# Kernel tuning notes

Hardware: AMD Instinct MI355X
Metric: run time of the kernel (lower is better)

Reference implementation:

```python
import jax, jax.numpy as jnp
import numpy as np

NUM_ITERATIONS = 3
LAMBDA_WEIGHT = 0.6
EPS = 1e-8


def _squash(s):
    # s: [N, out_dim]; norm over feature dim (dim=1 in torch, keepdim)
    s_norm = jnp.linalg.norm(s, axis=1, keepdims=True)
    scale = s_norm / (1.0 + s_norm)
    return scale * s / (s_norm + EPS)


def setup_inputs() -> dict:
    key = jax.random.key(0)
    k_h, k_adj, k_w, k_a = jax.random.split(key, 4)
    N, in_dim, out_dim = 4096, 128, 128
    h = jax.random.normal(k_h, (N, in_dim), dtype=jnp.float32)
    adj = jax.random.uniform(k_adj, (N, N), dtype=jnp.float32)
    # xavier_uniform for W [in_dim, out_dim] and attn_a [2*out_dim, 1]
    lim_w = float(np.sqrt(6.0 / (in_dim + out_dim)))
    W = jax.random.uniform(k_w, (in_dim, out_dim), minval=-lim_w, maxval=lim_w, dtype=jnp.float32)
    lim_a = float(np.sqrt(6.0 / (2 * out_dim + 1)))
    attn_a = jax.random.uniform(k_a, (2 * out_dim, 1), minval=-lim_a, maxval=lim_a, dtype=jnp.float32)
    return {"h": h, "adj": adj, "W": W, "attn_a": attn_a}


def reference(h, adj, W, attn_a):
    # Symmetric degree normalization
    d = adj.sum(axis=1) + 1e-8
    d_inv_sqrt = 1.0 / jnp.sqrt(d)
    adj_norm = d_inv_sqrt[:, None] * adj * d_inv_sqrt[None, :]  # [N, N]

    u_hat = h @ W  # [N, out_dim]

    # GAT-style scores via additive decomposition (same math as cat+matmul,
    # avoids the O(N^2 * 2d) h_concat tensor):
    out_dim = W.shape[1]
    a_src = attn_a[:out_dim, 0]  # [in_dim] (in_dim == out_dim)
    a_dst = attn_a[out_dim:, 0]
    attn_scores = (h @ a_src)[:, None] + (h @ a_dst)[None, :]  # [N, N]
    attn_weights = jax.nn.leaky_relu(attn_scores, negative_slope=0.2)

    # Dynamic routing
    b = adj_norm
    c = None
    for it in range(NUM_ITERATIONS):
        c = jax.nn.softmax(b, axis=1)  # [N, N]
        s = c @ u_hat                  # [N, out_dim]
        v = _squash(s)
        if it < NUM_ITERATIONS - 1:
            b = b + v @ u_hat.T        # agreement [N, N]

    combined = LAMBDA_WEIGHT * c + (1.0 - LAMBDA_WEIGHT) * jax.nn.softmax(attn_weights, axis=1)
    s = combined @ u_hat
    return _squash(s)
```

## Files before the change

kernel.cpp:

```cpp
#include <hip/hip_runtime.h>
#include <hip/hip_bf16.h>
#include <math.h>

#define N 4096
#define D 128
#define EPSV 1e-8f
#define KS 8

typedef __attribute__((ext_vector_type(8))) short bf16x8;
typedef __attribute__((ext_vector_type(4))) float f32x4;

__device__ __forceinline__ float lrelu(float x){ return x > 0.f ? x : 0.2f*x; }

__device__ __forceinline__ ushort bf16_hi(float x){
  __hip_bfloat16 h = __float2bfloat16(x);
  return *reinterpret_cast<ushort*>(&h);
}
__device__ __forceinline__ float bf16_tof(ushort u){
  __hip_bfloat16 h = *reinterpret_cast<__hip_bfloat16*>(&u);
  return __bfloat162float(h);
}

__device__ __forceinline__ float wave_sum(float v){
  #pragma unroll
  for (int off = 32; off; off >>= 1) v += __shfl_down(v, off);
  return v;
}
__device__ __forceinline__ float wave_max(float v){
  #pragma unroll
  for (int off = 32; off; off >>= 1) v = fmaxf(v, __shfl_down(v, off));
  return v;
}
__device__ __forceinline__ float block_sum256(float v, float* red){
  v = wave_sum(v);
  if ((threadIdx.x & 63) == 0) red[threadIdx.x >> 6] = v;
  __syncthreads();
  float r = (red[0] + red[1]) + (red[2] + red[3]);
  __syncthreads();
  return r;
}
__device__ __forceinline__ float block_max256(float v, float* red){
  v = wave_max(v);
  if ((threadIdx.x & 63) == 0) red[threadIdx.x >> 6] = v;
  __syncthreads();
  float r = fmaxf(fmaxf(red[0], red[1]), fmaxf(red[2], red[3]));
  __syncthreads();
  return r;
}

__global__ void k_rowsum(const float* __restrict__ adj, float* __restrict__ dis){
  int i = blockIdx.x;
  const float4* row = reinterpret_cast<const float4*>(adj + (size_t)i * N);
  float s = 0.f;
  #pragma unroll
  for (int l = 0; l < 4; ++l){
    float4 v = row[threadIdx.x + l * 256];
    s += (v.x + v.y) + (v.z + v.w);
  }
  __shared__ float red[4];
  s = block_sum256(s, red);
  if (threadIdx.x == 0) dis[i] = 1.0f / sqrtf(s + EPSV);
}

__global__ void k_uhat2(const float* __restrict__ h, const float* __restrict__ W,
                        const float* __restrict__ aa,
                        ushort* __restrict__ u_hi, ushort* __restrict__ u_lo,
                        float* __restrict__ p, float* __restrict__ q){
  int i = blockIdx.x, t = threadIdx.x;
  __shared__ float hs[D];
  __shared__ float red[4];
  float hv = h[(size_t)i * D + t];
  hs[t] = hv;
  __syncthreads();
  float acc = 0.f;
  #pragma unroll 8
  for (int k = 0; k < D; ++k) acc = fmaf(hs[k], W[k * D + t], acc);
  ushort hh = bf16_hi(acc);
  u_hi[(size_t)i * D + t] = hh;
  u_lo[(size_t)i * D + t] = bf16_hi(acc - bf16_tof(hh));
  float pv = hv * aa[t];
  float qv = hv * aa[D + t];
  pv = wave_sum(pv); qv = wave_sum(qv);
  if ((t & 63) == 0){ red[t >> 6] = pv; red[2 + (t >> 6)] = qv; }
  __syncthreads();
  if (t == 0){ p[i] = red[0] + red[1]; q[i] = red[2] + red[3]; }
}

__global__ void k_transposeU(const ushort* __restrict__ u_hi, const ushort* __restrict__ u_lo,
                             ushort* __restrict__ uT_hi, ushort* __restrict__ uT_lo){
  __shared__ ushort T[64][136];
  const int tid = threadIdx.x;
  const int j0 = blockIdx.x * 64;
  for (int pass = 0; pass < 2; ++pass){
    const ushort* s = pass ? u_lo : u_hi;
    ushort* d = pass ? uT_lo : uT_hi;
    __syncthreads();
    #pragma unroll
    for (int l = 0; l < 4; ++l){
      int r = l * 16 + (tid >> 4);
      int c = (tid & 15) * 8;
      *reinterpret_cast<uint4*>(&T[r][c]) =
          *reinterpret_cast<const uint4*>(s + (size_t)(j0 + r) * D + c);
    }
    __syncthreads();
    const int dd = tid >> 1, half = tid & 1;
    ushort* drow = d + (size_t)dd * N + j0 + half * 32;
    #pragma unroll
    for (int m4 = 0; m4 < 8; ++m4){
      ushort4 w;
      w.x = T[half * 32 + m4 * 4 + 0][dd];
      w.y = T[half * 32 + m4 * 4 + 1][dd];
      w.z = T[half * 32 + m4 * 4 + 2][dd];
      w.w = T[half * 32 + m4 * 4 + 3][dd];
      *reinterpret_cast<ushort4*>(drow + m4 * 4) = w;
    }
  }
}

template<int MODE>
__global__ void k_stats(const float* __restrict__ src, const float* __restrict__ dis,
                        const float* __restrict__ pv, const float* __restrict__ qv,
                        float* __restrict__ mb, float* __restrict__ lb,
                        float* __restrict__ ma, float* __restrict__ la){
  __shared__ float red[4];
  int i = blockIdx.x;
  const float4* src4 = reinterpret_cast<const float4*>(src + (size_t)i * N);
  const float4* dis4 = reinterpret_cast<const float4*>(dis);
  const float4* q4   = reinterpret_cast<const float4*>(qv);
  float di = (MODE == 0) ? dis[i] : 0.f;
  float pi = (MODE == 2) ? pv[i] : 0.f;
  float4 vals[4];
  float mx = -3.4e38f, amx = -3.4e38f;
  #pragma unroll
  for (int l = 0; l < 4; ++l){
    int t = threadIdx.x + l * 256;
    float4 a = src4[t];
    if (MODE == 0){
      float4 dj = dis4[t];
      a.x *= di * dj.x; a.y *= di * dj.y; a.z *= di * dj.z; a.w *= di * dj.w;
    }
    vals[l] = a;
    mx = fmaxf(mx, fmaxf(fmaxf(a.x, a.y), fmaxf(a.z, a.w)));
    if (MODE == 2){
      float4 qq = q4[t];
      float a0 = lrelu(pi + qq.x), a1 = lrelu(pi + qq.y);
      float a2 = lrelu(pi + qq.z), a3 = lrelu(pi + qq.w);
      amx = fmaxf(amx, fmaxf(fmaxf(a0, a1), fmaxf(a2, a3)));
    }
  }
  float m = block_max256(mx, red);
  float se = 0.f;
  #pragma unroll
  for (int l = 0; l < 4; ++l){
    float4 a = vals[l];
    se += expf(a.x - m) + expf(a.y - m) + expf(a.z - m) + expf(a.w - m);
  }
  float ls = block_sum256(se, red);
  if (MODE == 2){
    float am = block_max256(amx, red);
    float ase = 0.f;
    #pragma unroll
    for (int l = 0; l < 4; ++l){
      int t = threadIdx.x + l * 256;
      float4 qq = q4[t];
      ase += expf(lrelu(pi + qq.x) - am) + expf(lrelu(pi + qq.y) - am)
           + expf(lrelu(pi + qq.z) - am) + expf(lrelu(pi + qq.w) - am);
    }
    float al = block_sum256(ase, red);
    if (threadIdx.x == 0){ ma[i] = am; la[i] = al; }
  }
  if (threadIdx.x == 0){ mb[i] = m; lb[i] = ls; }
}

template<int MODE>
__global__ __launch_bounds__(256, 2)
void k_gemm3(const float* __restrict__ src, const float* __restrict__ dis,
             const float* __restrict__ p, const float* __restrict__ q,
             const float* __restrict__ mbv, const float* __restrict__ lbv,
             const float* __restrict__ mav, const float* __restrict__ lav,
             const ushort* __restrict__ uT_hi, const ushort* __restrict__ uT_lo,
             float* __restrict__ s_part)
{
  const int lane = threadIdx.x & 63;
  const int wave = threadIdx.x >> 6;
  const int row0 = blockIdx.x * 64 + wave * 16;
  const int cl   = lane & 15;
  const int kgrp = (lane >> 4) * 8;
  const int arow = row0 + cl;
  const int k0b  = blockIdx.y * (N / KS);

  const float mrow = mbv[arow];
  const float rl   = 1.0f / lbv[arow];
  const float dif  = (MODE == 0) ? dis[arow] : 0.f;
  float pi = 0.f, mar = 0.f, rla = 0.f;
  if (MODE == 2){ pi = p[arow]; mar = mav[arow]; rla = 1.0f / lav[arow]; }

  const float* arow_ptr = src + (size_t)arow * N;

  f32x4 acc[8] = {};

  for (int kt = 0; kt < N / KS; kt += 32){
    const int kk = k0b + kt + kgrp;
    bf16x8 bh[8], bl[8];
    #pragma unroll
    for (int ct = 0; ct < 8; ++ct){
      size_t off = (size_t)(ct * 16 + cl) * N + kk;
      bh[ct] = *reinterpret_cast<const bf16x8*>(uT_hi + off);
      bl[ct] = *reinterpret_cast<const bf16x8*>(uT_lo + off);
    }
    float av[8];
    *reinterpret_cast<float4*>(av)     = *reinterpret_cast<const float4*>(arow_ptr + kk);
    *reinterpret_cast<float4*>(av + 4) = *reinterpret_cast<const float4*>(arow_ptr + kk + 4);
    float ex[8];
    if (MODE == 0){
      float dv[8];
      *reinterpret_cast<float4*>(dv)     = *reinterpret_cast<const float4*>(dis + kk);
      *reinterpret_cast<float4*>(dv + 4) = *reinterpret_cast<const float4*>(dis + kk + 4);
      #pragma unroll
      for (int e = 0; e < 8; ++e) ex[e] = __expf(av[e] * dif * dv[e] - mrow) * rl;
    } else if (MODE == 1){
      #pragma unroll
      for (int e = 0; e < 8; ++e) ex[e] = __expf(av[e] - mrow) * rl;
    } else {
      float qv[8];
      *reinterpret_cast<float4*>(qv)     = *reinterpret_cast<const float4*>(q + kk);
      *reinterpret_cast<float4*>(qv + 4) = *reinterpret_cast<const float4*>(q + kk + 4);
      #pragma unroll
      for (int e = 0; e < 8; ++e){
        float c  = __expf(av[e] - mrow) * rl;
        float aw = __expf(lrelu(pi + qv[e]) - mar) * rla;
        ex[e] = 0.6f * c + 0.4f * aw;
      }
    }
    bf16x8 ahi, alo;
    #pragma unroll
    for (int e = 0; e < 8; ++e){
      ushort hh = bf16_hi(ex[e]);
      ahi[e] = (short)hh;
      alo[e] = (short)bf16_hi(ex[e] - bf16_tof(hh));
    }
    #pragma unroll
    for (int ct = 0; ct < 8; ++ct){
      acc[ct] = __builtin_amdgcn_mfma_f32_16x16x32_bf16(ahi, bh[ct], acc[ct], 0, 0, 0);
      acc[ct] = __builtin_amdgcn_mfma_f32_16x16x32_bf16(ahi, bl[ct], acc[ct], 0, 0, 0);
      acc[ct] = __builtin_amdgcn_mfma_f32_16x16x32_bf16(alo, bh[ct], acc[ct], 0, 0, 0);
    }
  }
  const int orow = row0 + (lane >> 4) * 4;
  float* sp = s_part + ((size_t)blockIdx.y * N + orow) * D + cl;
  #pragma unroll
  for (int ct = 0; ct < 8; ++ct)
    #pragma unroll
    for (int r = 0; r < 4; ++r)
      sp[(size_t)r * D + ct * 16] = acc[ct][r];
}

template<bool FINAL>
__global__ void k_reduce_squash2(const float* __restrict__ s_part, float* __restrict__ out,
                                 ushort* __restrict__ vh, ushort* __restrict__ vl){
  int row = blockIdx.x, t = threadIdx.x;
  float a = 0.f;
  #pragma unroll
  for (int y = 0; y < KS; ++y) a += s_part[((size_t)y * N + row) * D + t];
  __shared__ float red[2];
  float ss = wave_sum(a * a);
  if ((t & 63) == 0) red[t >> 6] = ss;
  __syncthreads();
  float tot = red[0] + red[1];
  float n = sqrtf(tot);
  float f = n / ((1.0f + n) * (n + EPSV));
  float val = a * f;
  if (FINAL) out[(size_t)row * D + t] = val;
  else {
    ushort hh = bf16_hi(val);
    vh[(size_t)row * D + t] = hh;
    vl[(size_t)row * D + t] = bf16_hi(val - bf16_tof(hh));
  }
}

template<bool FIRST>
__global__ __launch_bounds__(256, 4)
void k_bupd3(const ushort* __restrict__ v_hi, const ushort* __restrict__ v_lo,
             const ushort* __restrict__ u_hi, const ushort* __restrict__ u_lo,
             const float* __restrict__ adj, const float* __restrict__ dis,
             float* __restrict__ b)
{
  const int lane = threadIdx.x & 63;
  const int wave = threadIdx.x >> 6;
  const int row0 = (blockIdx.x >> 5) * 128 + wave * 32;
  const int col0 = (blockIdx.x & 31) * 128;
  const int cl   = lane & 15;
  const int kgrp = (lane >> 4) * 8;

  f32x4 acc[2][8] = {};

  #pragma unroll
  for (int ks = 0; ks < 4; ++ks){
    const int kk = ks * 32 + kgrp;
    bf16x8 a_h[2], a_l[2];
    #pragma unroll
    for (int rt = 0; rt < 2; ++rt){
      size_t off = (size_t)(row0 + rt * 16 + cl) * D + kk;
      a_h[rt] = *reinterpret_cast<const bf16x8*>(v_hi + off);
      a_l[rt] = *reinterpret_cast<const bf16x8*>(v_lo + off);
    }
    #pragma unroll
    for (int ct = 0; ct < 8; ++ct){
      size_t off = (size_t)(col0 + ct * 16 + cl) * D + kk;
      bf16x8 b_h = *reinterpret_cast<const bf16x8*>(u_hi + off);
      bf16x8 b_l = *reinterpret_cast<const bf16x8*>(u_lo + off);
      #pragma unroll
      for (int rt = 0; rt < 2; ++rt){
        acc[rt][ct] = __builtin_amdgcn_mfma_f32_16x16x32_bf16(a_h[rt], b_h, acc[rt][ct], 0, 0, 0);
        acc[rt][ct] = __builtin_amdgcn_mfma_f32_16x16x32_bf16(a_h[rt], b_l, acc[rt][ct], 0, 0, 0);
        acc[rt][ct] = __builtin_amdgcn_mfma_f32_16x16x32_bf16(a_l[rt], b_h, acc[rt][ct], 0, 0, 0);
      }
    }
  }

  float dcol[8];
  if (FIRST){
    #pragma unroll
    for (int ct = 0; ct < 8; ++ct) dcol[ct] = dis[col0 + ct * 16 + cl];
  }
  #pragma unroll
  for (int rt = 0; rt < 2; ++rt){
    const int orow = row0 + rt * 16 + (lane >> 4) * 4;
    #pragma unroll
    for (int r = 0; r < 4; ++r){
      const int gr = orow + r;
      const float drow = FIRST ? dis[gr] : 0.f;
      size_t base = (size_t)gr * N + col0 + cl;
      #pragma unroll
      for (int ct = 0; ct < 8; ++ct){
        size_t idx = base + ct * 16;
        if (FIRST) b[idx] = fmaf(adj[idx], drow * dcol[ct], acc[rt][ct][r]);
        else       b[idx] += acc[rt][ct][r];
      }
    }
  }
}

extern "C" void kernel_launch(void* const* d_in, const int* in_sizes, int n_in,
                              void* d_out, int out_size, void* d_ws, size_t ws_size,
                              hipStream_t stream) {
  const float* h   = (const float*)d_in[0];
  const float* adj = (const float*)d_in[1];
  const float* W   = (const float*)d_in[2];
  const float* aa  = (const float*)d_in[3];
  float* out = (float*)d_out;
  float* ws  = (float*)d_ws;

  float* dis = ws;
  float* p   = ws + 4096;
  float* q   = ws + 8192;
  float* mb  = ws + 12288;
  float* lb  = ws + 16384;
  float* ma  = ws + 20480;
  float* la  = ws + 24576;
  ushort* u_hi  = (ushort*)(ws + 32768);
  ushort* u_lo  = u_hi  + (size_t)N * D;
  ushort* uT_hi = u_lo  + (size_t)N * D;
  ushort* uT_lo = uT_hi + (size_t)N * D;
  ushort* v_hi  = uT_lo + (size_t)N * D;
  ushort* v_lo  = v_hi  + (size_t)N * D;
  float* b      = (float*)(v_lo + (size_t)N * D);
  float* s_part = b + (size_t)N * N;

  dim3 gg(64, KS);

  k_rowsum<<<N, 256, 0, stream>>>(adj, dis);
  k_uhat2<<<N, 128, 0, stream>>>(h, W, aa, u_hi, u_lo, p, q);
  k_transposeU<<<64, 256, 0, stream>>>(u_hi, u_lo, uT_hi, uT_lo);

  k_stats<0><<<N, 256, 0, stream>>>(adj, dis, p, q, mb, lb, ma, la);
  k_gemm3<0><<<gg, 256, 0, stream>>>(adj, dis, p, q, mb, lb, ma, la, uT_hi, uT_lo, s_part);
  k_reduce_squash2<false><<<N, 128, 0, stream>>>(s_part, out, v_hi, v_lo);
  k_bupd3<true><<<1024, 256, 0, stream>>>(v_hi, v_lo, u_hi, u_lo, adj, dis, b);

  k_stats<1><<<N, 256, 0, stream>>>(b, dis, p, q, mb, lb, ma, la);
  k_gemm3<1><<<gg, 256, 0, stream>>>(b, dis, p, q, mb, lb, ma, la, uT_hi, uT_lo, s_part);
  k_reduce_squash2<false><<<N, 128, 0, stream>>>(s_part, out, v_hi, v_lo);
  k_bupd3<false><<<1024, 256, 0, stream>>>(v_hi, v_lo, u_hi, u_lo, adj, dis, b);

  k_stats<2><<<N, 256, 0, stream>>>(b, dis, p, q, mb, lb, ma, la);
  k_gemm3<2><<<gg, 256, 0, stream>>>(b, dis, p, q, mb, lb, ma, la, uT_hi, uT_lo, s_part);
  k_reduce_squash2<true><<<N, 128, 0, stream>>>(s_part, out, v_hi, v_lo);
}
```

Measured before the change: 511.9 us.

## Fuse softmax normalization into routing GEMMs and drop separate stats passes

Removes the per-row max/sum stats kernels. Each GEMM now computes unnormalized exponentials and accumulates row sums, which the reduce kernel divides out afterwards. The attention softmax term gets its own GEMM pass up front, and the final combine happens in the last reduce. Other changes: the hi/lo bf16 U transpose is packed into an interleaved layout, the next A tile is prefetched, occupancy is raised to 4 blocks, and K-split depth is chosen from workspace size. Dropping max-subtraction saves a full N×N read per iteration but assumes routing logits stay small enough not to overflow exp.

```diff
diff --git a/kernel.cpp b/kernel.cpp
--- a/kernel.cpp
+++ b/kernel.cpp
@@ -5,7 +5,6 @@
 #define N 4096
 #define D 128
 #define EPSV 1e-8f
-#define KS 8
 
 typedef __attribute__((ext_vector_type(8))) short bf16x8;
 typedef __attribute__((ext_vector_type(4))) float f32x4;
@@ -26,24 +25,11 @@
   for (int off = 32; off; off >>= 1) v += __shfl_down(v, off);
   return v;
 }
-__device__ __forceinline__ float wave_max(float v){
-  #pragma unroll
-  for (int off = 32; off; off >>= 1) v = fmaxf(v, __shfl_down(v, off));
-  return v;
-}
 __device__ __forceinline__ float block_sum256(float v, float* red){
   v = wave_sum(v);
   if ((threadIdx.x & 63) == 0) red[threadIdx.x >> 6] = v;
   __syncthreads();
   float r = (red[0] + red[1]) + (red[2] + red[3]);
-  __syncthreads();
-  return r;
-}
-__device__ __forceinline__ float block_max256(float v, float* red){
-  v = wave_max(v);
-  if ((threadIdx.x & 63) == 0) red[threadIdx.x >> 6] = v;
-  __syncthreads();
-  float r = fmaxf(fmaxf(red[0], red[1]), fmaxf(red[2], red[3]));
   __syncthreads();
   return r;
 }
@@ -86,14 +72,13 @@
   if (t == 0){ p[i] = red[0] + red[1]; q[i] = red[2] + red[3]; }
 }
 
-__global__ void k_transposeU(const ushort* __restrict__ u_hi, const ushort* __restrict__ u_lo,
-                             ushort* __restrict__ uT_hi, ushort* __restrict__ uT_lo){
+__global__ void k_transposeU2(const ushort* __restrict__ u_hi, const ushort* __restrict__ u_lo,
+                              ushort* __restrict__ uT_pk){
   __shared__ ushort T[64][136];
   const int tid = threadIdx.x;
   const int j0 = blockIdx.x * 64;
   for (int pass = 0; pass < 2; ++pass){
     const ushort* s = pass ? u_lo : u_hi;
-    ushort* d = pass ? uT_lo : uT_hi;
     __syncthreads();
     #pragma unroll
     for (int l = 0; l < 4; ++l){
@@ -104,82 +89,26 @@
     }
     __syncthreads();
     const int dd = tid >> 1, half = tid & 1;
-    ushort* drow = d + (size_t)dd * N + j0 + half * 32;
-    #pragma unroll
-    for (int m4 = 0; m4 < 8; ++m4){
-      ushort4 w;
-      w.x = T[half * 32 + m4 * 4 + 0][dd];
-      w.y = T[half * 32 + m4 * 4 + 1][dd];
-      w.z = T[half * 32 + m4 * 4 + 2][dd];
-      w.w = T[half * 32 + m4 * 4 + 3][dd];
-      *reinterpret_cast<ushort4*>(drow + m4 * 4) = w;
+    #pragma unroll
+    for (int g = 0; g < 4; ++g){
+      int jb = half * 32 + g * 8;
+      uint w0 = (uint)T[jb+0][dd] | ((uint)T[jb+1][dd] << 16);
+      uint w1 = (uint)T[jb+2][dd] | ((uint)T[jb+3][dd] << 16);
+      uint w2 = (uint)T[jb+4][dd] | ((uint)T[jb+5][dd] << 16);
+      uint w3 = (uint)T[jb+6][dd] | ((uint)T[jb+7][dd] << 16);
+      uint4 w; w.x = w0; w.y = w1; w.z = w2; w.w = w3;
+      size_t off = ((size_t)dd * (N/8) + ((j0 + jb) >> 3)) * 16 + pass * 8;
+      *reinterpret_cast<uint4*>(uT_pk + off) = w;
     }
   }
 }
 
 template<int MODE>
-__global__ void k_stats(const float* __restrict__ src, const float* __restrict__ dis,
-                        const float* __restrict__ pv, const float* __restrict__ qv,
-                        float* __restrict__ mb, float* __restrict__ lb,
-                        float* __restrict__ ma, float* __restrict__ la){
-  __shared__ float red[4];
-  int i = blockIdx.x;
-  const float4* src4 = reinterpret_cast<const float4*>(src + (size_t)i * N);
-  const float4* dis4 = reinterpret_cast<const float4*>(dis);
-  const float4* q4   = reinterpret_cast<const float4*>(qv);
-  float di = (MODE == 0) ? dis[i] : 0.f;
-  float pi = (MODE == 2) ? pv[i] : 0.f;
-  float4 vals[4];
-  float mx = -3.4e38f, amx = -3.4e38f;
-  #pragma unroll
-  for (int l = 0; l < 4; ++l){
-    int t = threadIdx.x + l * 256;
-    float4 a = src4[t];
-    if (MODE == 0){
-      float4 dj = dis4[t];
-      a.x *= di * dj.x; a.y *= di * dj.y; a.z *= di * dj.z; a.w *= di * dj.w;
-    }
-    vals[l] = a;
-    mx = fmaxf(mx, fmaxf(fmaxf(a.x, a.y), fmaxf(a.z, a.w)));
-    if (MODE == 2){
-      float4 qq = q4[t];
-      float a0 = lrelu(pi + qq.x), a1 = lrelu(pi + qq.y);
-      float a2 = lrelu(pi + qq.z), a3 = lrelu(pi + qq.w);
-      amx = fmaxf(amx, fmaxf(fmaxf(a0, a1), fmaxf(a2, a3)));
-    }
-  }
-  float m = block_max256(mx, red);
-  float se = 0.f;
-  #pragma unroll
-  for (int l = 0; l < 4; ++l){
-    float4 a = vals[l];
-    se += expf(a.x - m) + expf(a.y - m) + expf(a.z - m) + expf(a.w - m);
-  }
-  float ls = block_sum256(se, red);
-  if (MODE == 2){
-    float am = block_max256(amx, red);
-    float ase = 0.f;
-    #pragma unroll
-    for (int l = 0; l < 4; ++l){
-      int t = threadIdx.x + l * 256;
-      float4 qq = q4[t];
-      ase += expf(lrelu(pi + qq.x) - am) + expf(lrelu(pi + qq.y) - am)
-           + expf(lrelu(pi + qq.z) - am) + expf(lrelu(pi + qq.w) - am);
-    }
-    float al = block_sum256(ase, red);
-    if (threadIdx.x == 0){ ma[i] = am; la[i] = al; }
-  }
-  if (threadIdx.x == 0){ mb[i] = m; lb[i] = ls; }
-}
-
-template<int MODE>
-__global__ __launch_bounds__(256, 2)
-void k_gemm3(const float* __restrict__ src, const float* __restrict__ dis,
+__global__ __launch_bounds__(256, 4)
+void k_gemm4(const float* __restrict__ src, const float* __restrict__ dis,
              const float* __restrict__ p, const float* __restrict__ q,
-             const float* __restrict__ mbv, const float* __restrict__ lbv,
-             const float* __restrict__ mav, const float* __restrict__ lav,
-             const ushort* __restrict__ uT_hi, const ushort* __restrict__ uT_lo,
-             float* __restrict__ s_part)
+             const ushort* __restrict__ uT_pk,
+             float* __restrict__ s_part, float* __restrict__ l_part, int kRange)
 {
   const int lane = threadIdx.x & 63;
   const int wave = threadIdx.x >> 6;
@@ -187,50 +116,47 @@
   const int cl   = lane & 15;
   const int kgrp = (lane >> 4) * 8;
   const int arow = row0 + cl;
-  const int k0b  = blockIdx.y * (N / KS);
-
-  const float mrow = mbv[arow];
-  const float rl   = 1.0f / lbv[arow];
-  const float dif  = (MODE == 0) ? dis[arow] : 0.f;
-  float pi = 0.f, mar = 0.f, rla = 0.f;
-  if (MODE == 2){ pi = p[arow]; mar = mav[arow]; rla = 1.0f / lav[arow]; }
-
-  const float* arow_ptr = src + (size_t)arow * N;
+  const int k0b  = blockIdx.y * kRange;
+
+  const float dif = (MODE == 0) ? dis[arow] : 0.f;
+  const float pi  = (MODE == 2) ? p[arow] : 0.f;
+  const float* srow = (MODE == 2) ? q : src + (size_t)arow * N;
 
   f32x4 acc[8] = {};
-
-  for (int kt = 0; kt < N / KS; kt += 32){
-    const int kk = k0b + kt + kgrp;
-    bf16x8 bh[8], bl[8];
-    #pragma unroll
-    for (int ct = 0; ct < 8; ++ct){
-      size_t off = (size_t)(ct * 16 + cl) * N + kk;
-      bh[ct] = *reinterpret_cast<const bf16x8*>(uT_hi + off);
-      bl[ct] = *reinterpret_cast<const bf16x8*>(uT_lo + off);
-    }
-    float av[8];
-    *reinterpret_cast<float4*>(av)     = *reinterpret_cast<const float4*>(arow_ptr + kk);
-    *reinterpret_cast<float4*>(av + 4) = *reinterpret_cast<const float4*>(arow_ptr + kk + 4);
-    float ex[8];
+  float lsum = 0.f;
+
+  float av[8], dv[8];
+  {
+    int kk = k0b + kgrp;
+    *reinterpret_cast<float4*>(av)     = *reinterpret_cast<const float4*>(srow + kk);
+    *reinterpret_cast<float4*>(av + 4) = *reinterpret_cast<const float4*>(srow + kk + 4);
     if (MODE == 0){
-      float dv[8];
       *reinterpret_cast<float4*>(dv)     = *reinterpret_cast<const float4*>(dis + kk);
       *reinterpret_cast<float4*>(dv + 4) = *reinterpret_cast<const float4*>(dis + kk + 4);
-      #pragma unroll
-      for (int e = 0; e < 8; ++e) ex[e] = __expf(av[e] * dif * dv[e] - mrow) * rl;
-    } else if (MODE == 1){
-      #pragma unroll
-      for (int e = 0; e < 8; ++e) ex[e] = __expf(av[e] - mrow) * rl;
-    } else {
-      float qv[8];
-      *reinterpret_cast<float4*>(qv)     = *reinterpret_cast<const float4*>(q + kk);
-      *reinterpret_cast<float4*>(qv + 4) = *reinterpret_cast<const float4*>(q + kk + 4);
-      #pragma unroll
-      for (int e = 0; e < 8; ++e){
-        float c  = __expf(av[e] - mrow) * rl;
-        float aw = __expf(lrelu(pi + qv[e]) - mar) * rla;
-        ex[e] = 0.6f * c + 0.4f * aw;
+    }
+  }
+
+  for (int kt = 0; kt < kRange; kt += 32){
+    const int kk = k0b + kt + kgrp;
+    float4 n0, n1, m0, m1;
+    const bool more = (kt + 32 < kRange);
+    if (more){
+      n0 = *reinterpret_cast<const float4*>(srow + kk + 32);
+      n1 = *reinterpret_cast<const float4*>(srow + kk + 36);
+      if (MODE == 0){
+        m0 = *reinterpret_cast<const float4*>(dis + kk + 32);
+        m1 = *reinterpret_cast<const float4*>(dis + kk + 36);
       }
+    }
+    float ex[8];
+    #pragma unroll
+    for (int e = 0; e < 8; ++e){
+      float x;
+      if (MODE == 0)      x = av[e] * dif * dv[e];
+      else if (MODE == 1) x = av[e];
+      else                x = lrelu(pi + av[e]);
+      ex[e] = __expf(x);
+      lsum += ex[e];
     }
     bf16x8 ahi, alo;
     #pragma unroll
@@ -239,13 +165,30 @@
       ahi[e] = (short)hh;
       alo[e] = (short)bf16_hi(ex[e] - bf16_tof(hh));
     }
+    const size_t kb16 = (size_t)(kk >> 3) * 16;
     #pragma unroll
     for (int ct = 0; ct < 8; ++ct){
-      acc[ct] = __builtin_amdgcn_mfma_f32_16x16x32_bf16(ahi, bh[ct], acc[ct], 0, 0, 0);
-      acc[ct] = __builtin_amdgcn_mfma_f32_16x16x32_bf16(ahi, bl[ct], acc[ct], 0, 0, 0);
-      acc[ct] = __builtin_amdgcn_mfma_f32_16x16x32_bf16(alo, bh[ct], acc[ct], 0, 0, 0);
-    }
-  }
+      const ushort* bp = uT_pk + (size_t)(ct * 16 + cl) * (N/8) * 16 + kb16;
+      bf16x8 bh = *reinterpret_cast<const bf16x8*>(bp);
+      bf16x8 bl = *reinterpret_cast<const bf16x8*>(bp + 8);
+      acc[ct] = __builtin_amdgcn_mfma_f32_16x16x32_bf16(ahi, bh, acc[ct], 0, 0, 0);
+      acc[ct] = __builtin_amdgcn_mfma_f32_16x16x32_bf16(ahi, bl, acc[ct], 0, 0, 0);
+      acc[ct] = __builtin_amdgcn_mfma_f32_16x16x32_bf16(alo, bh, acc[ct], 0, 0, 0);
+    }
+    if (more){
+      *reinterpret_cast<float4*>(av)     = n0;
+      *reinterpret_cast<float4*>(av + 4) = n1;
+      if (MODE == 0){
+        *reinterpret_cast<float4*>(dv)     = m0;
+        *reinterpret_cast<float4*>(dv + 4) = m1;
+      }
+    }
+  }
+
+  lsum += __shfl_xor(lsum, 16);
+  lsum += __shfl_xor(lsum, 32);
+  if (lane < 16) l_part[(size_t)blockIdx.y * N + row0 + lane] = lsum;
+
   const int orow = row0 + (lane >> 4) * 4;
   float* sp = s_part + ((size_t)blockIdx.y * N + orow) * D + cl;
   #pragma unroll
@@ -255,26 +198,52 @@
       sp[(size_t)r * D + ct * 16] = acc[ct][r];
 }
 
-template<bool FINAL>
-__global__ void k_reduce_squash2(const float* __restrict__ s_part, float* __restrict__ out,
-                                 ushort* __restrict__ vh, ushort* __restrict__ vl){
+__global__ void k_reduce_attn(const float* __restrict__ s_part, const float* __restrict__ l_part,
+                              float* __restrict__ s_attn, float* __restrict__ l_a, int ks){
   int row = blockIdx.x, t = threadIdx.x;
   float a = 0.f;
-  #pragma unroll
-  for (int y = 0; y < KS; ++y) a += s_part[((size_t)y * N + row) * D + t];
+  for (int y = 0; y < ks; ++y) a += s_part[((size_t)y * N + row) * D + t];
+  s_attn[(size_t)row * D + t] = a;
+  if (t == 0){
+    float la = 0.f;
+    for (int y = 0; y < ks; ++y) la += l_part[(size_t)y * N + row];
+    l_a[row] = la;
+  }
+}
+
+template<bool FINAL>
+__global__ void k_reduce_squash3(const float* __restrict__ s_part, const float* __restrict__ l_part,
+                                 const float* __restrict__ s_attn, const float* __restrict__ l_a,
+                                 float* __restrict__ out,
+                                 ushort* __restrict__ vh, ushort* __restrict__ vl, int ks){
+  int row = blockIdx.x, t = threadIdx.x;
+  float a = 0.f;
+  for (int y = 0; y < ks; ++y) a += s_part[((size_t)y * N + row) * D + t];
+  __shared__ float lbs;
   __shared__ float red[2];
-  float ss = wave_sum(a * a);
+  if (t == 0){
+    float lb = 0.f;
+    for (int y = 0; y < ks; ++y) lb += l_part[(size_t)y * N + row];
+    lbs = lb;
+  }
+  __syncthreads();
+  float val;
+  if (FINAL)
+    val = 0.6f * a / lbs + 0.4f * s_attn[(size_t)row * D + t] / l_a[row];
+  else
+    val = a / lbs;
+  float ss = wave_sum(val * val);
   if ((t & 63) == 0) red[t >> 6] = ss;
   __syncthreads();
   float tot = red[0] + red[1];
   float n = sqrtf(tot);
   float f = n / ((1.0f + n) * (n + EPSV));
-  float val = a * f;
-  if (FINAL) out[(size_t)row * D + t] = val;
+  float o = val * f;
+  if (FINAL) out[(size_t)row * D + t] = o;
   else {
-    ushort hh = bf16_hi(val);
+    ushort hh = bf16_hi(o);
     vh[(size_t)row * D + t] = hh;
-    vl[(size_t)row * D + t] = bf16_hi(val - bf16_tof(hh));
+    vl[(size_t)row * D + t] = bf16_hi(o - bf16_tof(hh));
   }
 }
 
@@ -351,39 +320,41 @@
   float* out = (float*)d_out;
   float* ws  = (float*)d_ws;
 
-  float* dis = ws;
-  float* p   = ws + 4096;
-  float* q   = ws + 8192;
-  float* mb  = ws + 12288;
-  float* lb  = ws + 16384;
-  float* ma  = ws + 20480;
-  float* la  = ws + 24576;
-  ushort* u_hi  = (ushort*)(ws + 32768);
+  float* dis    = ws;
+  float* p      = ws + 4096;
+  float* q      = ws + 8192;
+  float* l_a    = ws + 12288;
+  float* l_part = ws + 16384;
+  ushort* u_hi  = (ushort*)(ws + 81920);
   ushort* u_lo  = u_hi  + (size_t)N * D;
-  ushort* uT_hi = u_lo  + (size_t)N * D;
-  ushort* uT_lo = uT_hi + (size_t)N * D;
-  ushort* v_hi  = uT_lo + (size_t)N * D;
+  ushort* uT_pk = u_lo  + (size_t)N * D;
+  ushort* v_hi  = uT_pk + (size_t)(N/8) * D * 16;
   ushort* v_lo  = v_hi  + (size_t)N * D;
-  float* b      = (float*)(v_lo + (size_t)N * D);
+  float* s_attn = (float*)(v_lo + (size_t)N * D);
+  float* b      = s_attn + (size_t)N * D;
   float* s_part = b + (size_t)N * N;
 
+  size_t base_floats = (size_t)(s_part - ws);
+  int KS = 16;
+  while (KS > 1 && (base_floats + (size_t)KS * N * D) * 4 > ws_size) KS >>= 1;
+  int kRange = N / KS;
   dim3 gg(64, KS);
 
   k_rowsum<<<N, 256, 0, stream>>>(adj, dis);
   k_uhat2<<<N, 128, 0, stream>>>(h, W, aa, u_hi, u_lo, p, q);
-  k_transposeU<<<64, 256, 0, stream>>>(u_hi, u_lo, uT_hi, uT_lo);
-
-  k_stats<0><<<N, 256, 0, stream>>>(adj, dis, p, q, mb, lb, ma, la);
-  k_gemm3<0><<<gg, 256, 0, stream>>>(adj, dis, p, q, mb, lb, ma, la, uT_hi, uT_lo, s_part);
-  k_reduce_squash2<false><<<N, 128, 0, stream>>>(s_part, out, v_hi, v_lo);
+  k_transposeU2<<<64, 256, 0, stream>>>(u_hi, u_lo, uT_pk);
+
+  k_gemm4<2><<<gg, 256, 0, stream>>>(nullptr, dis, p, q, uT_pk, s_part, l_part, kRange);
+  k_reduce_attn<<<N, 128, 0, stream>>>(s_part, l_part, s_attn, l_a, KS);
+
+  k_gemm4<0><<<gg, 256, 0, stream>>>(adj, dis, p, q, uT_pk, s_part, l_part, kRange);
+  k_reduce_squash3<false><<<N, 128, 0, stream>>>(s_part, l_part, s_attn, l_a, out, v_hi, v_lo, KS);
   k_bupd3<true><<<1024, 256, 0, stream>>>(v_hi, v_lo, u_hi, u_lo, adj, dis, b);
 
-  k_stats<1><<<N, 256, 0, stream>>>(b, dis, p, q, mb, lb, ma, la);
-  k_gemm3<1><<<gg, 256, 0, stream>>>(b, dis, p, q, mb, lb, ma, la, uT_hi, uT_lo, s_part);
-  k_reduce_squash2<false><<<N, 128, 0, stream>>>(s_part, out, v_hi, v_lo);
+  k_gemm4<1><<<gg, 256, 0, stream>>>(b, dis, p, q, uT_pk, s_part, l_part, kRange);
+  k_reduce_squash3<false><<<N, 128, 0, stream>>>(s_part, l_part, s_attn, l_a, out, v_hi, v_lo, KS);
   k_bupd3<false><<<1024, 256, 0, stream>>>(v_hi, v_lo, u_hi, u_lo, adj, dis, b);
 
-  k_stats<2><<<N, 256, 0, stream>>>(b, dis, p, q, mb, lb, ma, la);
-  k_gemm3<2><<<gg, 256, 0, stream>>>(b, dis, p, q, mb, lb, ma, la, uT_hi, uT_lo, s_part);
-  k_reduce_squash2<true><<<N, 128, 0, stream>>>(s_part, out, v_hi, v_lo);
-}
+  k_gemm4<1><<<gg, 256, 0, stream>>>(b, dis, p, q, uT_pk, s_part, l_part, kRange);
+  k_reduce_squash3<true><<<N, 128, 0, stream>>>(s_part, l_part, s_attn, l_a, out, v_hi, v_lo, KS);
+}
```

New measurement: 552.2 us. 1.08x slower.
